# Kernel tuning notes

Measured on AMD Instinct MI355X. Metric: run time of the kernel, lower is better.

Reference implementation:

```python
import jax, jax.numpy as jnp
import numpy as np

B, H, W = 2, 128, 128
MID = 64            # mid_channels
DG = 16             # deform_groups
MAX_RES = 10.0      # max_residue_magnitude
CIN_OFF = 3 * MID + 4   # 196: cat(extra_feat, flow_1, flow_2)
COFF = DG * 27          # 432: o1 + o2 + mask, each DG*9


def setup_inputs() -> dict:
    key = jax.random.key(0)
    ks = jax.random.split(key, 9)
    return {
        "extra_feat": jax.random.normal(ks[0], (B, 3 * MID, H, W), jnp.float32),
        "flow_1": jax.random.normal(ks[1], (B, 2, H, W), jnp.float32) * 2.0,
        "flow_2": jax.random.normal(ks[2], (B, 2, H, W), jnp.float32) * 2.0,
        "feat_prop": jax.random.normal(ks[3], (B, MID, H, W), jnp.float32),
        "feat_n2": jax.random.normal(ks[4], (B, MID, H, W), jnp.float32),
        "w_off": jax.random.normal(ks[5], (COFF, CIN_OFF, 3, 3), jnp.float32) * 0.02,
        "b_off": jax.random.normal(ks[6], (COFF,), jnp.float32) * 0.02,
        "dc_weight": jax.random.normal(ks[7], (MID, 2 * MID, 3, 3), jnp.float32) * 0.05,
        "dc_bias": jax.random.normal(ks[8], (MID,), jnp.float32) * 0.05,
    }


def _conv3x3(x, w, b):
    y = jax.lax.conv_general_dilated(
        x, w, window_strides=(1, 1), padding=((1, 1), (1, 1)),
        dimension_numbers=("NCHW", "OIHW", "NCHW"))
    return y + b[None, :, None, None]


def _deform_conv2d(inp, offset, mask, weight, bias):
    # inp: [B, Cin, H, W]; offset: [B, 2*DG*9, H, W] (per group, per kernel pos: (dy, dx));
    # mask: [B, DG*9, H, W]; weight: [Cout, Cin, 3, 3]; stride=1, pad=1, dil=1.
    Bb, Cin, Hi, Wi = inp.shape
    K = 9
    cg = Cin // DG
    Ho, Wo = Hi, Wi
    ki = jnp.repeat(jnp.arange(3), 3)  # kernel row index per flat k (row-major)
    kj = jnp.tile(jnp.arange(3), 3)
    base_y = (jnp.arange(Ho) - 1)[None, :, None] + ki[:, None, None]  # [K, Ho, 1]
    base_x = (jnp.arange(Wo) - 1)[None, None, :] + kj[:, None, None]  # [K, 1, Wo]
    off = offset.reshape(Bb, DG, K, 2, Ho, Wo)
    py = base_y[None, None] + off[:, :, :, 0]  # [B, DG, K, Ho, Wo]
    px = base_x[None, None] + off[:, :, :, 1]
    y0 = jnp.floor(py)
    x0 = jnp.floor(px)
    inp_g = inp.reshape(Bb, DG, cg, Hi * Wi)
    acc = jnp.zeros((Bb, DG, cg, K, Ho, Wo), inp.dtype)
    for dy in (0.0, 1.0):
        for dx in (0.0, 1.0):
            yc = y0 + dy
            xc = x0 + dx
            wgt = (1.0 - jnp.abs(py - yc)) * (1.0 - jnp.abs(px - xc))
            valid = (yc >= 0) & (yc < Hi) & (xc >= 0) & (xc < Wi)
            idx = (jnp.clip(yc, 0, Hi - 1) * Wi + jnp.clip(xc, 0, Wi - 1)).astype(jnp.int32)
            idx = jnp.broadcast_to(idx.reshape(Bb, DG, 1, K * Ho * Wo), (Bb, DG, cg, K * Ho * Wo))
            g = jnp.take_along_axis(inp_g, idx, axis=3).reshape(Bb, DG, cg, K, Ho, Wo)
            acc = acc + g * (wgt * valid)[:, :, None]
    sm = acc * mask.reshape(Bb, DG, 1, K, Ho, Wo)  # modulated samples
    wr = weight.reshape(weight.shape[0], DG, cg, K)
    out = jnp.einsum("bgckhw,ogck->bohw", sm, wr) + bias[None, :, None, None]
    return out


def reference(extra_feat, flow_1, flow_2, feat_prop, feat_n2, w_off, b_off, dc_weight, dc_bias):
    x = jnp.concatenate([extra_feat, flow_1, flow_2], axis=1)
    out = _conv3x3(x, w_off, b_off)
    o1, o2, m = jnp.split(out, 3, axis=1)  # each [B, DG*9, H, W]
    offset = MAX_RES * jnp.tanh(jnp.concatenate([o1, o2], axis=1))
    rep = DG * 3 * 3 // 2  # 72
    f1 = jnp.tile(flow_1[:, ::-1], (1, rep, 1, 1))  # flip(1): (dx,dy)->(dy,dx)
    f2 = jnp.tile(flow_2[:, ::-1], (1, rep, 1, 1))
    half = offset.shape[1] // 2
    offset = jnp.concatenate([offset[:, :half] + f1, offset[:, half:] + f2], axis=1)
    mask = jax.nn.sigmoid(m)
    inp = jnp.concatenate([feat_prop, feat_n2], axis=1)
    return _deform_conv2d(inp, offset, mask, dc_weight, dc_bias)
```

## Files before the change

kernel.cpp:

```cpp
#include <hip/hip_runtime.h>
#include <math.h>

#define Hh 128
#define Ww 128
#define HW (128*128)
#define CIN_OFF 196
#define COFF 432

typedef _Float16 half8 __attribute__((ext_vector_type(8)));
typedef _Float16 half4 __attribute__((ext_vector_type(4)));
typedef _Float16 half2v __attribute__((ext_vector_type(2)));
typedef float f32x4 __attribute__((ext_vector_type(4)));

static __device__ __forceinline__ half8 splat8(float v) {
  _Float16 h = (_Float16)v;
  half8 r = {h, h, h, h, h, h, h, h};
  return r;
}

__global__ __launch_bounds__(256) void k_prep_all(
    const float* __restrict__ dcw, const float* __restrict__ w_off,
    const float* __restrict__ fp, const float* __restrict__ fn2,
    _Float16* __restrict__ wH, _Float16* __restrict__ BpT, _Float16* __restrict__ Bt,
    _Float16* __restrict__ featT) {
  const int bid = blockIdx.x;
  if (bid < 3375) {
    const int idx = bid * 256 + (int)threadIdx.x;
    if (idx < 73728) {
      const int co = idx / 1152;
      const int j  = idx - co * 1152;
      const int k  = j >> 7;
      const int ci = j & 127;
      wH[idx] = (_Float16)dcw[(co * 128 + ci) * 9 + k];
    } else if (idx < 73728 + 774144) {
      const int j  = idx - 73728;
      const int c  = j & 7;
      const int n  = (j >> 3) % 448;
      const int sl = (j >> 3) / 448;
      const int l4 = sl & 3;
      const int s  = sl >> 2;
      const int t  = s / 6;
      const int cg = s - t * 6;
      const int ci = cg * 32 + l4 * 8 + c;
      BpT[j] = (_Float16)((n < COFF) ? w_off[((size_t)n * CIN_OFF + ci) * 9 + t] : 0.f);
    } else {
      const int j = idx - 73728 - 774144;
      const int c = j & 3;
      const int n = (j >> 2) % 448;
      const int t = (j >> 2) / 448;
      Bt[j] = (_Float16)((n < COFF) ? w_off[((size_t)n * CIN_OFF + 192 + c) * 9 + t] : 0.f);
    }
  } else {
    const int t = (bid - 3375) * 256 + (int)threadIdx.x;
    const int b = t >> 14;
    const int hw = t & 16383;
#pragma unroll
    for (int g = 0; g < 16; ++g) {
      const float* src = (g < 8) ? fp : fn2;
      const int ch0 = (g & 7) * 8;
      half8 v;
#pragma unroll
      for (int c = 0; c < 8; ++c)
        v[c] = (_Float16)src[(size_t)(b * 64 + ch0 + c) * HW + hw];
      *(half8*)(featT + (((size_t)(b * 16 + g)) * HW + hw) * 8) = v;
    }
  }
}

__global__ __launch_bounds__(1024, 4) void k_offconv_mfma(
    const float* __restrict__ extra, const float* __restrict__ f1, const float* __restrict__ f2,
    const _Float16* __restrict__ BpT, const _Float16* __restrict__ Bt,
    const float* __restrict__ b_off,
    _Float16* __restrict__ off_pm, _Float16* __restrict__ mask_pm) {
  __shared__ __align__(16) _Float16 smA[3 * 130 * 192];
  __shared__ __align__(16) _Float16 smT[3 * 130 * 4];
  const int h    = blockIdx.x;
  const int b    = blockIdx.y;
  const int tid  = (int)threadIdx.x;
  const int lane = tid & 63;
  const int wid  = tid >> 6;
  const int wm   = wid & 3;
  const int wn   = wid >> 2;
  const int m_base = wm * 32;
  const int n_base = wn * 112;
  const int l15 = lane & 15;
  const int l4  = lane >> 4;

  if (tid < 588) {
    const int p2 = tid % 98;
    const int rr = tid / 98;
    const int r  = (rr >= 3) ? (rr - 3) : rr;
    const int px = (rr >= 3) ? 129 : 0;
    if (p2 < 96) {
      const int ci = 2 * p2, biw = ci >> 3;
      const int sw = ((biw & 24) | ((biw & 7) ^ (px & 7))) << 3;
      *(half2v*)(smA + (r * 130 + px) * 192 + sw + (ci & 7)) = (half2v){(_Float16)0.f, (_Float16)0.f};
    } else {
      *(half2v*)(smT + (r * 130 + px) * 4 + 2 * (p2 - 96)) = (half2v){(_Float16)0.f, (_Float16)0.f};
    }
  }

#pragma unroll 3
  for (int j = 0; j < 9; ++j) {
    const int J   = tid + 1024 * j;
    const int p2a = J & 15;
    const int qa  = (J >> 4) & 3;
    const int R   = J >> 6;
    const int r   = R / 48;
    const int rem = R - 48 * r;
    const int qh  = rem & 7;
    const int p2h = rem >> 3;
    const int q   = qa + 4 * qh;
    const int p2  = p2a + 16 * p2h;
    const int ci  = 2 * p2;
    const int gh  = h - 1 + r;
    float4 va = {0.f, 0.f, 0.f, 0.f}, vb = va;
    if ((unsigned)gh < (unsigned)Hh) {
      const float* xp = extra + (size_t)(b * 192 + ci) * HW + gh * Ww + 4 * q;
      va = *(const float4*)xp;
      vb = *(const float4*)(xp + HW);
    }
    const float av[4] = {va.x, va.y, va.z, va.w};
    const float bv[4] = {vb.x, vb.y, vb.z, vb.w};
    const int biw = p2 >> 2;
#pragma unroll
    for (int i = 0; i < 4; ++i) {
      const int px = 1 + 4 * q + i;
      const int sw = ((biw & 24) | ((biw & 7) ^ (px & 7))) << 3;
      half2v pk; pk[0] = (_Float16)av[i]; pk[1] = (_Float16)bv[i];
      *(half2v*)(smA + (r * 130 + px) * 192 + sw + (ci & 7)) = pk;
    }
  }
  if (tid < 192) {
    const int q   = tid & 31;
    const int p2t = (tid >> 5) & 1;
    const int r   = tid >> 6;
    const int gh  = h - 1 + r;
    float4 va = {0.f, 0.f, 0.f, 0.f}, vb = va;
    if ((unsigned)gh < (unsigned)Hh) {
      const float* xp = (p2t ? f2 : f1) + (size_t)(b * 2) * HW + gh * Ww + 4 * q;
      va = *(const float4*)xp;
      vb = *(const float4*)(xp + HW);
    }
    const float av[4] = {va.x, va.y, va.z, va.w};
    const float bv[4] = {vb.x, vb.y, vb.z, vb.w};
#pragma unroll
    for (int i = 0; i < 4; ++i) {
      const int px = 1 + 4 * q + i;
      half2v pk; pk[0] = (_Float16)av[i]; pk[1] = (_Float16)bv[i];
      *(half2v*)(smT + (r * 130 + px) * 4 + 2 * p2t) = pk;
    }
  }
  __syncthreads();

  f32x4 acc[2][7];
#pragma unroll
  for (int i = 0; i < 2; ++i)
#pragma unroll
    for (int j = 0; j < 7; ++j) acc[i][j] = (f32x4){0.f, 0.f, 0.f, 0.f};

  const bool lz = (l4 == 0);
#pragma unroll 3
  for (int t = 0; t < 9; ++t) {
    const int ki = t / 3;
    const int kj = t - 3 * ki;
#pragma unroll
    for (int cg = 0; cg < 6; ++cg) {
      const int s4 = ((t * 6 + cg) * 4 + l4) * 448;
      half8 bf[7];
#pragma unroll
      for (int f = 0; f < 7; ++f)
        bf[f] = *(const half8*)(BpT + (size_t)(s4 + n_base + f * 16 + l15) * 8);
      half8 af[2];
#pragma unroll
      for (int mf = 0; mf < 2; ++mf) {
        const int px = m_base + mf * 16 + l15 + kj;
        const int bi = cg * 4 + l4;
        af[mf] = *(const half8*)(smA + (ki * 130 + px) * 192 +
                                 (((bi & 24) | ((bi & 7) ^ (px & 7))) << 3));
      }
#pragma unroll
      for (int mf = 0; mf < 2; ++mf)
#pragma unroll
        for (int f = 0; f < 7; ++f)
          acc[mf][f] = __builtin_amdgcn_mfma_f32_16x16x32_f16(af[mf], bf[f], acc[mf][f], 0, 0, 0);
    }
    half8 aft[2];
#pragma unroll
    for (int mf = 0; mf < 2; ++mf) {
      const int px = m_base + mf * 16 + l15 + kj;
      const half4 tv = *(const half4*)(smT + (ki * 130 + px) * 4);
      half8 a = {0, 0, 0, 0, 0, 0, 0, 0};
      if (lz) { a[0] = tv[0]; a[1] = tv[1]; a[2] = tv[2]; a[3] = tv[3]; }
      aft[mf] = a;
    }
#pragma unroll
    for (int f = 0; f < 7; ++f) {
      const half4 wv = *(const half4*)(Bt + (size_t)(t * 448 + n_base + f * 16 + l15) * 4);
      half8 bb = {0, 0, 0, 0, 0, 0, 0, 0};
      if (lz) { bb[0] = wv[0]; bb[1] = wv[1]; bb[2] = wv[2]; bb[3] = wv[3]; }
#pragma unroll
      for (int mf = 0; mf < 2; ++mf)
        acc[mf][f] = __builtin_amdgcn_mfma_f32_16x16x32_f16(aft[mf], bb, acc[mf][f], 0, 0, 0);
    }
  }

  __syncthreads();
  _Float16* so = smA;
  const int hw0 = h * Ww;
#pragma unroll
  for (int f = 0; f < 7; ++f) {
    const int n = n_base + f * 16 + l15;
    const float bias = (n < COFF) ? b_off[n] : 0.f;
    const bool isOff = (n < 288);
    const float* fl = (n < 144) ? f1 : f2;
    const size_t fladd = (size_t)(b * 2 + ((n & 1) ^ 1)) * HW;
#pragma unroll
    for (int mf = 0; mf < 2; ++mf) {
#pragma unroll
      for (int rr = 0; rr < 4; ++rr) {
        const int px = m_base + mf * 16 + l4 * 4 + rr;
        const float v = acc[mf][f][rr] + bias;
        float val;
        if (isOff) {
          const float e = __expf(2.f * v);
          val = 10.f * (1.f - 2.f / (e + 1.f)) + fl[fladd + hw0 + px];
        } else {
          val = 1.f / (1.f + __expf(-v));
        }
        so[px * 456 + n] = (_Float16)val;
      }
    }
  }
  __syncthreads();
  for (int T = tid; T < 4608; T += 1024) {
    const int px = T / 36, c = T - px * 36;
    const half8 v = *(const half8*)(so + px * 456 + c * 8);
    *(half8*)(off_pm + ((size_t)b * HW + hw0 + px) * 288 + c * 8) = v;
  }
  for (int T = tid; T < 2304; T += 1024) {
    const int px = T / 18, c = T - px * 18;
    const half8 v = *(const half8*)(so + px * 456 + 288 + c * 8);
    *(half8*)(mask_pm + ((size_t)b * HW + hw0 + px) * 144 + c * 8) = v;
  }
}

__global__ __launch_bounds__(256, 4) void k_deform2(
    const _Float16* __restrict__ featT, const _Float16* __restrict__ off_pm,
    const _Float16* __restrict__ mask_pm, const _Float16* __restrict__ wH,
    const float* __restrict__ dcb, float* __restrict__ out) {
  __shared__ __align__(16) char smem[16 * 1160 * 2];
  _Float16* sm = (_Float16*)smem;
  float* red = (float*)smem;
  const int w0  = blockIdx.x * 16;
  const int h   = blockIdx.y;
  const int b   = blockIdx.z;
  const int tid = (int)threadIdx.x;
  const int lane = tid & 63, wid = tid >> 6;
  const int l15 = lane & 15, l4 = lane >> 4;

#pragma unroll 3
  for (int i = 0; i < 9; ++i) {
    const int p   = tid + i * 256;
    const int pix = p / 144;
    const int r   = p - pix * 144;
    const int g   = r / 9;
    const int k   = r - g * 9;
    const int w   = w0 + pix;
    const int hw  = h * Ww + w;
    const half2v offh = *(const half2v*)(off_pm + ((size_t)b * HW + hw) * 288 + 2 * r);
    const float mk = (float)mask_pm[((size_t)b * HW + hw) * 144 + r];
    const int ki = (k >= 6) ? 2 : (k >= 3 ? 1 : 0);
    const int kj = k - 3 * ki;
    const float py = (float)(h - 1 + ki) + (float)offh[0];
    const float px = (float)(w - 1 + kj) + (float)offh[1];
    const float y0f = floorf(py), x0f = floorf(px);
    const int y0 = (int)y0f, x0 = (int)x0f;
    const float ly = py - y0f, lx = px - x0f;
    const float hy = 1.f - ly, hx = 1.f - lx;
    const int y1 = y0 + 1, x1 = x0 + 1;
    const bool vy0 = (unsigned)y0 < (unsigned)Hh, vy1 = (unsigned)y1 < (unsigned)Hh;
    const bool vx0 = (unsigned)x0 < (unsigned)Ww, vx1 = (unsigned)x1 < (unsigned)Ww;
    const float w00 = (vy0 && vx0) ? hy * hx : 0.f;
    const float w01 = (vy0 && vx1) ? hy * lx : 0.f;
    const float w10 = (vy1 && vx0) ? ly * hx : 0.f;
    const float w11 = (vy1 && vx1) ? ly * lx : 0.f;
    const int cy0 = min(max(y0, 0), Hh - 1), cy1 = min(max(y1, 0), Hh - 1);
    const int cx0 = min(max(x0, 0), Ww - 1), cx1 = min(max(x1, 0), Ww - 1);
    const _Float16* gbase = featT + ((size_t)(b * 16 + g) * HW) * 8;
    const half8 s00 = *(const half8*)(gbase + (cy0 * Ww + cx0) * 8);
    const half8 s01 = *(const half8*)(gbase + (cy0 * Ww + cx1) * 8);
    const half8 s10 = *(const half8*)(gbase + (cy1 * Ww + cx0) * 8);
    const half8 s11 = *(const half8*)(gbase + (cy1 * Ww + cx1) * 8);
    half8 v = s00 * splat8(w00) + s01 * splat8(w01) + s10 * splat8(w10) + s11 * splat8(w11);
    v = v * splat8(mk);
    const int swz = (g ^ (k & 7)) << 3;
    *(half8*)(sm + pix * 1160 + k * 128 + swz) = v;
  }
  __syncthreads();

  f32x4 acc[4];
#pragma unroll
  for (int nf = 0; nf < 4; ++nf) acc[nf] = (f32x4){0.f, 0.f, 0.f, 0.f};
#pragma unroll
  for (int j = 0; j < 9; ++j) {
    const int s  = wid * 9 + j;
    const int k  = s >> 2;
    const int cg = s & 3;
    const int gidx = cg * 4 + l4;
    const half8 af = *(const half8*)(sm + l15 * 1160 + k * 128 + ((gidx ^ (k & 7)) << 3));
    const int koff = s * 32 + l4 * 8;
#pragma unroll
    for (int nf = 0; nf < 4; ++nf) {
      const half8 bf = *(const half8*)(wH + (nf * 16 + l15) * 1152 + koff);
      acc[nf] = __builtin_amdgcn_mfma_f32_16x16x32_f16(af, bf, acc[nf], 0, 0, 0);
    }
  }
  __syncthreads();
#pragma unroll
  for (int nf = 0; nf < 4; ++nf)
#pragma unroll
    for (int rr = 0; rr < 4; ++rr)
      red[(wid * 16 + l4 * 4 + rr) * 66 + nf * 16 + l15] = acc[nf][rr];
  __syncthreads();

  const int m  = tid & 15;
  const int ng = tid >> 4;
#pragma unroll
  for (int i = 0; i < 4; ++i) {
    const int n = ng + 16 * i;
    float val = red[(0 * 16 + m) * 66 + n] + red[(1 * 16 + m) * 66 + n] +
                red[(2 * 16 + m) * 66 + n] + red[(3 * 16 + m) * 66 + n];
    out[(size_t)(b * 64 + n) * HW + h * Ww + w0 + m] = val + dcb[n];
  }
}

extern "C" void kernel_launch(void* const* d_in, const int* in_sizes, int n_in,
                              void* d_out, int out_size, void* d_ws, size_t ws_size,
                              hipStream_t stream) {
  const float* extra = (const float*)d_in[0];
  const float* f1    = (const float*)d_in[1];
  const float* f2    = (const float*)d_in[2];
  const float* fp    = (const float*)d_in[3];
  const float* fn2   = (const float*)d_in[4];
  const float* w_off = (const float*)d_in[5];
  const float* b_off = (const float*)d_in[6];
  const float* dcw   = (const float*)d_in[7];
  const float* dcb   = (const float*)d_in[8];
  float* out = (float*)d_out;

  _Float16* off_pm  = (_Float16*)d_ws;
  _Float16* mask_pm = off_pm + (size_t)2 * 288 * HW;
  _Float16* featT   = mask_pm + (size_t)2 * 144 * HW;
  _Float16* BpT     = featT + (size_t)2 * 128 * HW;
  _Float16* Bt      = BpT + 774144;
  _Float16* wH      = Bt + 16128;

  hipLaunchKernelGGL(k_prep_all, dim3(3503), dim3(256), 0, stream,
                     dcw, w_off, fp, fn2, wH, BpT, Bt, featT);
  hipLaunchKernelGGL(k_offconv_mfma, dim3(128, 2), dim3(1024), 0, stream,
                     extra, f1, f2, BpT, Bt, b_off, off_pm, mask_pm);
  hipLaunchKernelGGL(k_deform2, dim3(8, 128, 2), dim3(256), 0, stream,
                     featT, off_pm, mask_pm, wH, dcb, out);
}
```

Before: 183.3 us.

## Software-pipeline offset-conv MFMA loads and prefetch deform offsets/masks

```diff
diff --git a/kernel.cpp b/kernel.cpp
--- a/kernel.cpp
+++ b/kernel.cpp
@@ -67,7 +67,7 @@
   }
 }
 
-__global__ __launch_bounds__(1024, 4) void k_offconv_mfma(
+__global__ __launch_bounds__(1024, 3) void k_offconv_mfma(
     const float* __restrict__ extra, const float* __restrict__ f1, const float* __restrict__ f2,
     const _Float16* __restrict__ BpT, const _Float16* __restrict__ Bt,
     const float* __restrict__ b_off,
@@ -159,32 +159,49 @@
 #pragma unroll
     for (int j = 0; j < 7; ++j) acc[i][j] = (f32x4){0.f, 0.f, 0.f, 0.f};
 
+  auto loadB = [&](half8* dst, int s) {
+    const int base = (s * 4 + l4) * 448 + n_base + l15;
+#pragma unroll
+    for (int f = 0; f < 7; ++f)
+      dst[f] = *(const half8*)(BpT + (size_t)(base + f * 16) * 8);
+  };
+  auto loadA = [&](half8* dst, int s) {
+    const int t  = s / 6, cg = s - 6 * t;
+    const int ki = t / 3, kj = t - 3 * ki;
+    const int bi = cg * 4 + l4;
+#pragma unroll
+    for (int mf = 0; mf < 2; ++mf) {
+      const int px = m_base + mf * 16 + l15 + kj;
+      dst[mf] = *(const half8*)(smA + (ki * 130 + px) * 192 +
+                                (((bi & 24) | ((bi & 7) ^ (px & 7))) << 3));
+    }
+  };
+  auto domfma = [&](const half8* af, const half8* bf) {
+#pragma unroll
+    for (int mf = 0; mf < 2; ++mf)
+#pragma unroll
+      for (int f = 0; f < 7; ++f)
+        acc[mf][f] = __builtin_amdgcn_mfma_f32_16x16x32_f16(af[mf], bf[f], acc[mf][f], 0, 0, 0);
+  };
+
+  half8 bfA[7], bfB[7], afA[2], afB[2];
+  loadB(bfA, 0); loadA(afA, 0);
+#pragma unroll 3
+  for (int sp = 0; sp < 26; ++sp) {
+    loadB(bfB, 2 * sp + 1); loadA(afB, 2 * sp + 1);
+    domfma(afA, bfA);
+    loadB(bfA, 2 * sp + 2); loadA(afA, 2 * sp + 2);
+    domfma(afB, bfB);
+  }
+  loadB(bfB, 53); loadA(afB, 53);
+  domfma(afA, bfA);
+  domfma(afB, bfB);
+
   const bool lz = (l4 == 0);
 #pragma unroll 3
   for (int t = 0; t < 9; ++t) {
     const int ki = t / 3;
     const int kj = t - 3 * ki;
-#pragma unroll
-    for (int cg = 0; cg < 6; ++cg) {
-      const int s4 = ((t * 6 + cg) * 4 + l4) * 448;
-      half8 bf[7];
-#pragma unroll
-      for (int f = 0; f < 7; ++f)
-        bf[f] = *(const half8*)(BpT + (size_t)(s4 + n_base + f * 16 + l15) * 8);
-      half8 af[2];
-#pragma unroll
-      for (int mf = 0; mf < 2; ++mf) {
-        const int px = m_base + mf * 16 + l15 + kj;
-        const int bi = cg * 4 + l4;
-        af[mf] = *(const half8*)(smA + (ki * 130 + px) * 192 +
-                                 (((bi & 24) | ((bi & 7) ^ (px & 7))) << 3));
-      }
-#pragma unroll
-      for (int mf = 0; mf < 2; ++mf)
-#pragma unroll
-        for (int f = 0; f < 7; ++f)
-          acc[mf][f] = __builtin_amdgcn_mfma_f32_16x16x32_f16(af[mf], bf[f], acc[mf][f], 0, 0, 0);
-    }
     half8 aft[2];
 #pragma unroll
     for (int mf = 0; mf < 2; ++mf) {
@@ -259,7 +276,19 @@
   const int lane = tid & 63, wid = tid >> 6;
   const int l15 = lane & 15, l4 = lane >> 4;
 
-#pragma unroll 3
+  half2v offv[9];
+  _Float16 mkv[9];
+#pragma unroll
+  for (int i = 0; i < 9; ++i) {
+    const int p   = tid + i * 256;
+    const int pix = p / 144;
+    const int r   = p - pix * 144;
+    const int w   = w0 + pix;
+    const int hw  = h * Ww + w;
+    offv[i] = *(const half2v*)(off_pm + ((size_t)b * HW + hw) * 288 + 2 * r);
+    mkv[i]  = mask_pm[((size_t)b * HW + hw) * 144 + r];
+  }
+#pragma unroll
   for (int i = 0; i < 9; ++i) {
     const int p   = tid + i * 256;
     const int pix = p / 144;
@@ -267,13 +296,11 @@
     const int g   = r / 9;
     const int k   = r - g * 9;
     const int w   = w0 + pix;
-    const int hw  = h * Ww + w;
-    const half2v offh = *(const half2v*)(off_pm + ((size_t)b * HW + hw) * 288 + 2 * r);
-    const float mk = (float)mask_pm[((size_t)b * HW + hw) * 144 + r];
+    const float mk = (float)mkv[i];
     const int ki = (k >= 6) ? 2 : (k >= 3 ? 1 : 0);
     const int kj = k - 3 * ki;
-    const float py = (float)(h - 1 + ki) + (float)offh[0];
-    const float px = (float)(w - 1 + kj) + (float)offh[1];
+    const float py = (float)(h - 1 + ki) + (float)offv[i][0];
+    const float px = (float)(w - 1 + kj) + (float)offv[i][1];
     const float y0f = floorf(py), x0f = floorf(px);
     const int y0 = (int)y0f, x0 = (int)x0f;
     const float ly = py - y0f, lx = px - x0f;
```

New measurement: 187.9 us. 1.03x slower.

## Fuse offset conv and deformable conv into one kernel via shared memory

Applied to the files above, without the earlier changes.

```diff
diff --git a/kernel.cpp b/kernel.cpp
--- a/kernel.cpp
+++ b/kernel.cpp
@@ -67,11 +67,12 @@
   }
 }
 
-__global__ __launch_bounds__(1024, 4) void k_offconv_mfma(
+__global__ __launch_bounds__(1024, 4) void k_fused(
     const float* __restrict__ extra, const float* __restrict__ f1, const float* __restrict__ f2,
     const _Float16* __restrict__ BpT, const _Float16* __restrict__ Bt,
     const float* __restrict__ b_off,
-    _Float16* __restrict__ off_pm, _Float16* __restrict__ mask_pm) {
+    const _Float16* __restrict__ featT, const _Float16* __restrict__ wH,
+    const float* __restrict__ dcb, float* __restrict__ out) {
   __shared__ __align__(16) _Float16 smA[3 * 130 * 192];
   __shared__ __align__(16) _Float16 smT[3 * 130 * 4];
   const int h    = blockIdx.x;
@@ -207,14 +208,13 @@
 
   __syncthreads();
   _Float16* so = smA;
-  const int hw0 = h * Ww;
 #pragma unroll
   for (int f = 0; f < 7; ++f) {
     const int n = n_base + f * 16 + l15;
     const float bias = (n < COFF) ? b_off[n] : 0.f;
     const bool isOff = (n < 288);
     const float* fl = (n < 144) ? f1 : f2;
-    const size_t fladd = (size_t)(b * 2 + ((n & 1) ^ 1)) * HW;
+    const size_t fladd = (size_t)(b * 2 + ((n & 1) ^ 1)) * HW + h * Ww;
 #pragma unroll
     for (int mf = 0; mf < 2; ++mf) {
 #pragma unroll
@@ -224,7 +224,7 @@
         float val;
         if (isOff) {
           const float e = __expf(2.f * v);
-          val = 10.f * (1.f - 2.f / (e + 1.f)) + fl[fladd + hw0 + px];
+          val = 10.f * (1.f - 2.f / (e + 1.f)) + fl[fladd + px];
         } else {
           val = 1.f / (1.f + __expf(-v));
         }
@@ -233,47 +233,27 @@
     }
   }
   __syncthreads();
-  for (int T = tid; T < 4608; T += 1024) {
-    const int px = T / 36, c = T - px * 36;
-    const half8 v = *(const half8*)(so + px * 456 + c * 8);
-    *(half8*)(off_pm + ((size_t)b * HW + hw0 + px) * 288 + c * 8) = v;
-  }
-  for (int T = tid; T < 2304; T += 1024) {
-    const int px = T / 18, c = T - px * 18;
-    const half8 v = *(const half8*)(so + px * 456 + 288 + c * 8);
-    *(half8*)(mask_pm + ((size_t)b * HW + hw0 + px) * 144 + c * 8) = v;
-  }
-}
-
-__global__ __launch_bounds__(256, 4) void k_deform2(
-    const _Float16* __restrict__ featT, const _Float16* __restrict__ off_pm,
-    const _Float16* __restrict__ mask_pm, const _Float16* __restrict__ wH,
-    const float* __restrict__ dcb, float* __restrict__ out) {
-  __shared__ __align__(16) char smem[16 * 1160 * 2];
-  _Float16* sm = (_Float16*)smem;
-  float* red = (float*)smem;
-  const int w0  = blockIdx.x * 16;
-  const int h   = blockIdx.y;
-  const int b   = blockIdx.z;
-  const int tid = (int)threadIdx.x;
-  const int lane = tid & 63, wid = tid >> 6;
-  const int l15 = lane & 15, l4 = lane >> 4;
+
+  const int kh  = wid & 1;
+  const int mf8 = wid >> 1;
+  const int pxc = mf8 * 16 + l15;
+  f32x4 pacc[4];
+#pragma unroll
+  for (int nf = 0; nf < 4; ++nf) pacc[nf] = (f32x4){0.f, 0.f, 0.f, 0.f};
 
 #pragma unroll 3
-  for (int i = 0; i < 9; ++i) {
-    const int p   = tid + i * 256;
-    const int pix = p / 144;
-    const int r   = p - pix * 144;
-    const int g   = r / 9;
-    const int k   = r - g * 9;
-    const int w   = w0 + pix;
-    const int hw  = h * Ww + w;
-    const half2v offh = *(const half2v*)(off_pm + ((size_t)b * HW + hw) * 288 + 2 * r);
-    const float mk = (float)mask_pm[((size_t)b * HW + hw) * 144 + r];
+  for (int j = 0; j < 18; ++j) {
+    const int s  = kh * 18 + j;
+    const int k  = s >> 2;
+    const int cg = s & 3;
+    const int g  = cg * 4 + l4;
+    const int r  = g * 9 + k;
+    const half2v od = *(const half2v*)(so + pxc * 456 + 2 * r);
+    const float mk = (float)so[pxc * 456 + 288 + r];
     const int ki = (k >= 6) ? 2 : (k >= 3 ? 1 : 0);
     const int kj = k - 3 * ki;
-    const float py = (float)(h - 1 + ki) + (float)offh[0];
-    const float px = (float)(w - 1 + kj) + (float)offh[1];
+    const float py = (float)(h - 1 + ki) + (float)od[0];
+    const float px = (float)(pxc - 1 + kj) + (float)od[1];
     const float y0f = floorf(py), x0f = floorf(px);
     const int y0 = (int)y0f, x0 = (int)x0f;
     const float ly = py - y0f, lx = px - x0f;
@@ -292,46 +272,32 @@
     const half8 s01 = *(const half8*)(gbase + (cy0 * Ww + cx1) * 8);
     const half8 s10 = *(const half8*)(gbase + (cy1 * Ww + cx0) * 8);
     const half8 s11 = *(const half8*)(gbase + (cy1 * Ww + cx1) * 8);
-    half8 v = s00 * splat8(w00) + s01 * splat8(w01) + s10 * splat8(w10) + s11 * splat8(w11);
-    v = v * splat8(mk);
-    const int swz = (g ^ (k & 7)) << 3;
-    *(half8*)(sm + pix * 1160 + k * 128 + swz) = v;
-  }
-  __syncthreads();
-
-  f32x4 acc[4];
-#pragma unroll
-  for (int nf = 0; nf < 4; ++nf) acc[nf] = (f32x4){0.f, 0.f, 0.f, 0.f};
-#pragma unroll
-  for (int j = 0; j < 9; ++j) {
-    const int s  = wid * 9 + j;
-    const int k  = s >> 2;
-    const int cg = s & 3;
-    const int gidx = cg * 4 + l4;
-    const half8 af = *(const half8*)(sm + l15 * 1160 + k * 128 + ((gidx ^ (k & 7)) << 3));
+    half8 af = s00 * splat8(w00) + s01 * splat8(w01) + s10 * splat8(w10) + s11 * splat8(w11);
+    af = af * splat8(mk);
     const int koff = s * 32 + l4 * 8;
 #pragma unroll
     for (int nf = 0; nf < 4; ++nf) {
-      const half8 bf = *(const half8*)(wH + (nf * 16 + l15) * 1152 + koff);
-      acc[nf] = __builtin_amdgcn_mfma_f32_16x16x32_f16(af, bf, acc[nf], 0, 0, 0);
-    }
-  }
-  __syncthreads();
+      const half8 bf = *(const half8*)(wH + (size_t)(nf * 16 + l15) * 1152 + koff);
+      pacc[nf] = __builtin_amdgcn_mfma_f32_16x16x32_f16(af, bf, pacc[nf], 0, 0, 0);
+    }
+  }
+  __syncthreads();
+  float* red = (float*)smA;
 #pragma unroll
   for (int nf = 0; nf < 4; ++nf)
 #pragma unroll
     for (int rr = 0; rr < 4; ++rr)
-      red[(wid * 16 + l4 * 4 + rr) * 66 + nf * 16 + l15] = acc[nf][rr];
-  __syncthreads();
-
-  const int m  = tid & 15;
-  const int ng = tid >> 4;
-#pragma unroll
-  for (int i = 0; i < 4; ++i) {
-    const int n = ng + 16 * i;
-    float val = red[(0 * 16 + m) * 66 + n] + red[(1 * 16 + m) * 66 + n] +
-                red[(2 * 16 + m) * 66 + n] + red[(3 * 16 + m) * 66 + n];
-    out[(size_t)(b * 64 + n) * HW + h * Ww + w0 + m] = val + dcb[n];
+      red[(wid * 16 + l4 * 4 + rr) * 66 + nf * 16 + l15] = pacc[nf][rr];
+  __syncthreads();
+
+  for (int T = tid; T < 8192; T += 1024) {
+    const int px2 = T & 127;
+    const int n   = T >> 7;
+    const int mfr = px2 >> 4;
+    const int pxl = px2 & 15;
+    const float val = red[((mfr * 2 + 0) * 16 + pxl) * 66 + n] +
+                      red[((mfr * 2 + 1) * 16 + pxl) * 66 + n];
+    out[(size_t)(b * 64 + n) * HW + h * Ww + px2] = val + dcb[n];
   }
 }
 
@@ -349,17 +315,13 @@
   const float* dcb   = (const float*)d_in[8];
   float* out = (float*)d_out;
 
-  _Float16* off_pm  = (_Float16*)d_ws;
-  _Float16* mask_pm = off_pm + (size_t)2 * 288 * HW;
-  _Float16* featT   = mask_pm + (size_t)2 * 144 * HW;
-  _Float16* BpT     = featT + (size_t)2 * 128 * HW;
-  _Float16* Bt      = BpT + 774144;
-  _Float16* wH      = Bt + 16128;
+  _Float16* featT = (_Float16*)d_ws;
+  _Float16* BpT   = featT + (size_t)2 * 128 * HW;
+  _Float16* Bt    = BpT + 774144;
+  _Float16* wH    = Bt + 16128;
 
   hipLaunchKernelGGL(k_prep_all, dim3(3503), dim3(256), 0, stream,
                      dcw, w_off, fp, fn2, wH, BpT, Bt, featT);
-  hipLaunchKernelGGL(k_offconv_mfma, dim3(128, 2), dim3(1024), 0, stream,
-                     extra, f1, f2, BpT, Bt, b_off, off_pm, mask_pm);
-  hipLaunchKernelGGL(k_deform2, dim3(8, 128, 2), dim3(256), 0, stream,
-                     featT, off_pm, mask_pm, wH, dcb, out);
+  hipLaunchKernelGGL(k_fused, dim3(128, 2), dim3(1024), 0, stream,
+                     extra, f1, f2, BpT, Bt, b_off, featT, wH, dcb, out);
 }
```

New measurement: 188.2 us. +2.7%, slower.

## Enlarge per-wave tile in offset conv and prefetch offsets in deform kernel

Applied to the files above, without the earlier changes.

```diff
diff --git a/kernel.cpp b/kernel.cpp
--- a/kernel.cpp
+++ b/kernel.cpp
@@ -67,7 +67,7 @@
   }
 }
 
-__global__ __launch_bounds__(1024, 4) void k_offconv_mfma(
+__global__ __launch_bounds__(512, 2) void k_offconv_mfma(
     const float* __restrict__ extra, const float* __restrict__ f1, const float* __restrict__ f2,
     const _Float16* __restrict__ BpT, const _Float16* __restrict__ Bt,
     const float* __restrict__ b_off,
@@ -79,16 +79,16 @@
   const int tid  = (int)threadIdx.x;
   const int lane = tid & 63;
   const int wid  = tid >> 6;
-  const int wm   = wid & 3;
-  const int wn   = wid >> 2;
-  const int m_base = wm * 32;
+  const int wm   = wid & 1;
+  const int wn   = (wid >> 1) & 3;
+  const int m_base = wm * 64;
   const int n_base = wn * 112;
   const int l15 = lane & 15;
   const int l4  = lane >> 4;
 
-  if (tid < 588) {
-    const int p2 = tid % 98;
-    const int rr = tid / 98;
+  for (int z = tid; z < 588; z += 512) {
+    const int p2 = z % 98;
+    const int rr = z / 98;
     const int r  = (rr >= 3) ? (rr - 3) : rr;
     const int px = (rr >= 3) ? 129 : 0;
     if (p2 < 96) {
@@ -101,8 +101,8 @@
   }
 
 #pragma unroll 3
-  for (int j = 0; j < 9; ++j) {
-    const int J   = tid + 1024 * j;
+  for (int j = 0; j < 18; ++j) {
+    const int J   = tid + 512 * j;
     const int p2a = J & 15;
     const int qa  = (J >> 4) & 3;
     const int R   = J >> 6;
@@ -153,9 +153,9 @@
   }
   __syncthreads();
 
-  f32x4 acc[2][7];
-#pragma unroll
-  for (int i = 0; i < 2; ++i)
+  f32x4 acc[4][7];
+#pragma unroll
+  for (int i = 0; i < 4; ++i)
 #pragma unroll
     for (int j = 0; j < 7; ++j) acc[i][j] = (f32x4){0.f, 0.f, 0.f, 0.f};
 
@@ -171,23 +171,23 @@
 #pragma unroll
       for (int f = 0; f < 7; ++f)
         bf[f] = *(const half8*)(BpT + (size_t)(s4 + n_base + f * 16 + l15) * 8);
-      half8 af[2];
-#pragma unroll
-      for (int mf = 0; mf < 2; ++mf) {
+      half8 af[4];
+#pragma unroll
+      for (int mf = 0; mf < 4; ++mf) {
         const int px = m_base + mf * 16 + l15 + kj;
         const int bi = cg * 4 + l4;
         af[mf] = *(const half8*)(smA + (ki * 130 + px) * 192 +
                                  (((bi & 24) | ((bi & 7) ^ (px & 7))) << 3));
       }
 #pragma unroll
-      for (int mf = 0; mf < 2; ++mf)
+      for (int mf = 0; mf < 4; ++mf)
 #pragma unroll
         for (int f = 0; f < 7; ++f)
           acc[mf][f] = __builtin_amdgcn_mfma_f32_16x16x32_f16(af[mf], bf[f], acc[mf][f], 0, 0, 0);
     }
-    half8 aft[2];
-#pragma unroll
-    for (int mf = 0; mf < 2; ++mf) {
+    half8 aft[4];
+#pragma unroll
+    for (int mf = 0; mf < 4; ++mf) {
       const int px = m_base + mf * 16 + l15 + kj;
       const half4 tv = *(const half4*)(smT + (ki * 130 + px) * 4);
       half8 a = {0, 0, 0, 0, 0, 0, 0, 0};
@@ -200,7 +200,7 @@
       half8 bb = {0, 0, 0, 0, 0, 0, 0, 0};
       if (lz) { bb[0] = wv[0]; bb[1] = wv[1]; bb[2] = wv[2]; bb[3] = wv[3]; }
 #pragma unroll
-      for (int mf = 0; mf < 2; ++mf)
+      for (int mf = 0; mf < 4; ++mf)
         acc[mf][f] = __builtin_amdgcn_mfma_f32_16x16x32_f16(aft[mf], bb, acc[mf][f], 0, 0, 0);
     }
   }
@@ -214,9 +214,9 @@
     const float bias = (n < COFF) ? b_off[n] : 0.f;
     const bool isOff = (n < 288);
     const float* fl = (n < 144) ? f1 : f2;
-    const size_t fladd = (size_t)(b * 2 + ((n & 1) ^ 1)) * HW;
-#pragma unroll
-    for (int mf = 0; mf < 2; ++mf) {
+    const size_t fladd = (size_t)(b * 2 + ((n & 1) ^ 1)) * HW + hw0;
+#pragma unroll
+    for (int mf = 0; mf < 4; ++mf) {
 #pragma unroll
       for (int rr = 0; rr < 4; ++rr) {
         const int px = m_base + mf * 16 + l4 * 4 + rr;
@@ -224,7 +224,7 @@
         float val;
         if (isOff) {
           const float e = __expf(2.f * v);
-          val = 10.f * (1.f - 2.f / (e + 1.f)) + fl[fladd + hw0 + px];
+          val = 10.f * (1.f - 2.f / (e + 1.f)) + fl[fladd + px];
         } else {
           val = 1.f / (1.f + __expf(-v));
         }
@@ -233,12 +233,12 @@
     }
   }
   __syncthreads();
-  for (int T = tid; T < 4608; T += 1024) {
+  for (int T = tid; T < 4608; T += 512) {
     const int px = T / 36, c = T - px * 36;
     const half8 v = *(const half8*)(so + px * 456 + c * 8);
     *(half8*)(off_pm + ((size_t)b * HW + hw0 + px) * 288 + c * 8) = v;
   }
-  for (int T = tid; T < 2304; T += 1024) {
+  for (int T = tid; T < 2304; T += 512) {
     const int px = T / 18, c = T - px * 18;
     const half8 v = *(const half8*)(so + px * 456 + 288 + c * 8);
     *(half8*)(mask_pm + ((size_t)b * HW + hw0 + px) * 144 + c * 8) = v;
@@ -259,7 +259,19 @@
   const int lane = tid & 63, wid = tid >> 6;
   const int l15 = lane & 15, l4 = lane >> 4;
 
-#pragma unroll 3
+  half2v offv[9];
+  _Float16 mkv[9];
+#pragma unroll
+  for (int i = 0; i < 9; ++i) {
+    const int p   = tid + i * 256;
+    const int pix = p / 144;
+    const int r   = p - pix * 144;
+    const int w   = w0 + pix;
+    const int hw  = h * Ww + w;
+    offv[i] = *(const half2v*)(off_pm + ((size_t)b * HW + hw) * 288 + 2 * r);
+    mkv[i]  = mask_pm[((size_t)b * HW + hw) * 144 + r];
+  }
+#pragma unroll
   for (int i = 0; i < 9; ++i) {
     const int p   = tid + i * 256;
     const int pix = p / 144;
@@ -267,13 +279,11 @@
     const int g   = r / 9;
     const int k   = r - g * 9;
     const int w   = w0 + pix;
-    const int hw  = h * Ww + w;
-    const half2v offh = *(const half2v*)(off_pm + ((size_t)b * HW + hw) * 288 + 2 * r);
-    const float mk = (float)mask_pm[((size_t)b * HW + hw) * 144 + r];
+    const float mk = (float)mkv[i];
     const int ki = (k >= 6) ? 2 : (k >= 3 ? 1 : 0);
     const int kj = k - 3 * ki;
-    const float py = (float)(h - 1 + ki) + (float)offh[0];
-    const float px = (float)(w - 1 + kj) + (float)offh[1];
+    const float py = (float)(h - 1 + ki) + (float)offv[i][0];
+    const float px = (float)(w - 1 + kj) + (float)offv[i][1];
     const float y0f = floorf(py), x0f = floorf(px);
     const int y0 = (int)y0f, x0 = (int)x0f;
     const float ly = py - y0f, lx = px - x0f;
@@ -358,7 +368,7 @@
 
   hipLaunchKernelGGL(k_prep_all, dim3(3503), dim3(256), 0, stream,
                      dcw, w_off, fp, fn2, wH, BpT, Bt, featT);
-  hipLaunchKernelGGL(k_offconv_mfma, dim3(128, 2), dim3(1024), 0, stream,
+  hipLaunchKernelGGL(k_offconv_mfma, dim3(128, 2), dim3(512), 0, stream,
                      extra, f1, f2, BpT, Bt, b_off, off_pm, mask_pm);
   hipLaunchKernelGGL(k_deform2, dim3(8, 128, 2), dim3(256), 0, stream,
                      featT, off_pm, mask_pm, wH, dcb, out);
```

Result: no change. 185.1 us (+1.0%).
